# Performance work log

Measured on AMD Instinct MI355X. Metric: run time of the kernel, lower is better.

Reference implementation:

```python
import jax, jax.numpy as jnp
import numpy as np

D_IN = 1024
D_OUT = 1024
NUM_HEADS = 16
HEAD_DIM = D_OUT // NUM_HEADS


def setup_inputs() -> dict:
    key = jax.random.key(0)
    k1, k2, k3, k4 = jax.random.split(key, 4)
    x = jax.random.normal(k1, (2, 2048, D_IN), dtype=jnp.float32)
    # Linear weights stored torch-style [out_features, in_features]
    W_qkv = jax.random.normal(k2, (3 * D_OUT, D_IN), dtype=jnp.float32) * (1.0 / np.sqrt(D_IN))
    W_out = jax.random.normal(k3, (D_OUT, D_OUT), dtype=jnp.float32) * (1.0 / np.sqrt(D_OUT))
    b_out = jax.random.normal(k4, (D_OUT,), dtype=jnp.float32) * 0.01
    return {"x": x, "W_qkv": W_qkv, "W_out": W_out, "b_out": b_out}


def reference(x, W_qkv, W_out, b_out):
    b, s, _ = x.shape
    qkv = jnp.einsum('bsi,oi->bso', x, W_qkv)  # [b, s, 3*d_out]
    q, k, v = jnp.split(qkv, 3, axis=-1)
    def to_heads(t):
        return t.reshape(b, s, NUM_HEADS, HEAD_DIM).transpose(0, 2, 1, 3)
    q, k, v = to_heads(q), to_heads(k), to_heads(v)
    # NOTE: original module does NOT scale by 1/sqrt(head_dim)
    scores = jnp.einsum('bhqd,bhkd->bhqk', q, k)
    causal = jnp.tril(jnp.ones((s, s), dtype=bool))  # True = keep
    scores = jnp.where(causal[None, None], scores, -jnp.inf)
    attn = jax.nn.softmax(scores, axis=-1)
    ctx = jnp.einsum('bhqk,bhkd->bhqd', attn, v)
    ctx = ctx.transpose(0, 2, 1, 3).reshape(b, s, D_OUT)
    return jnp.einsum('bso,po->bsp', ctx, W_out) + b_out
```

## Files before the change

### kernel.cpp

```cpp
#include <hip/hip_runtime.h>
#include <cstdint>
#include <cstddef>


typedef __attribute__((ext_vector_type(8))) short bf16x8;
typedef __attribute__((ext_vector_type(4))) float f32x4;

#define LOG2E 1.44269504f

#define MFMA16(a, b, c) __builtin_amdgcn_mfma_f32_16x16x32_bf16((a), (b), (c), 0, 0, 0)

#define GLDS16(g, s)                                                        \
  __builtin_amdgcn_global_load_lds(                                         \
      (const __attribute__((address_space(1))) void*)(g),                   \
      (__attribute__((address_space(3))) void*)(s), 16, 0, 0)

#if __has_builtin(__builtin_amdgcn_exp2f)
#define EXP2F(x) __builtin_amdgcn_exp2f(x)
#else
#define EXP2F(x) exp2f(x)
#endif

static __device__ __forceinline__ unsigned short f2bf(float f) {
  unsigned int u = __builtin_bit_cast(unsigned int, f);
  u += 0x7FFFu + ((u >> 16) & 1u);
  return (unsigned short)(u >> 16);
}

static __device__ __forceinline__ unsigned int pk2bf(float a, float b) {
  const unsigned int ua = __builtin_bit_cast(unsigned int, a) + 0x8000u;
  const unsigned int ub = __builtin_bit_cast(unsigned int, b) + 0x8000u;
  return __builtin_amdgcn_perm(ub, ua, 0x07060302);
}

__global__ __launch_bounds__(256) void cast_bf16(const float* __restrict__ x,
                                                 const float* __restrict__ wq,
                                                 const float* __restrict__ wo,
                                                 unsigned short* __restrict__ xb,
                                                 unsigned short* __restrict__ wqb,
                                                 unsigned short* __restrict__ wob)
{
  const int id = blockIdx.x * 256 + threadIdx.x;
  const float* src;
  unsigned short* dst;
  int off;
  if (id < 1048576)               { src = x;  dst = xb;  off = id; }
  else if (id < 1048576 + 786432) { src = wq; dst = wqb; off = id - 1048576; }
  else                            { src = wo; dst = wob; off = id - (1048576 + 786432); }
  float4 v = ((const float4*)src)[off];
  ushort4 o;
  o.x = f2bf(v.x); o.y = f2bf(v.y); o.z = f2bf(v.z); o.w = f2bf(v.w);
  ((ushort4*)dst)[off] = o;
}

template <int MODE>
__global__ __launch_bounds__(256) void gemm_bt(const unsigned short* __restrict__ A,
                                               const unsigned short* __restrict__ B,
                                               const float* __restrict__ bias,
                                               float* __restrict__ OutF,
                                               unsigned short* __restrict__ Qb,
                                               unsigned short* __restrict__ Kb,
                                               unsigned short* __restrict__ Vt)
{
  __shared__ unsigned short pool[9216];
  unsigned short* Asm = pool;
  unsigned short* Bsm = pool + 4096;

  const int tid  = threadIdx.x;
  const int wave = tid >> 6, lane = tid & 63, quad = lane >> 4, cl = lane & 15;
  const int wm = wave >> 1, wn = wave & 1;
  const int m0 = blockIdx.y * 128, n0 = blockIdx.x * 128;
  const int sr = lane >> 2, sc = lane & 3;

  f32x4 acc[4][4];
  #pragma unroll
  for (int i = 0; i < 4; ++i)
    #pragma unroll
    for (int j = 0; j < 4; ++j)
      #pragma unroll
      for (int r = 0; r < 4; ++r) acc[i][j][r] = 0.f;

  const int scs = (sc ^ ((sr >> 1) & 3)) * 8;
  const int rchunk = (quad ^ ((cl >> 1) & 3)) * 8;
  for (int k0 = 0; k0 < 1024; k0 += 32) {
    __syncthreads();
    #pragma unroll
    for (int ii = 0; ii < 2; ++ii) {
      const int r = wave * 32 + ii * 16 + sr;
      GLDS16(A + (size_t)(m0 + r) * 1024 + k0 + scs, &Asm[(wave * 32 + ii * 16) * 32]);
      GLDS16(B + (size_t)(n0 + r) * 1024 + k0 + scs, &Bsm[(wave * 32 + ii * 16) * 32]);
    }
    __syncthreads();

    bf16x8 af[4], bfr[4];
    #pragma unroll
    for (int mt = 0; mt < 4; ++mt)
      af[mt] = *(const bf16x8*)&Asm[(wm * 64 + mt * 16 + cl) * 32 + rchunk];
    #pragma unroll
    for (int nt = 0; nt < 4; ++nt)
      bfr[nt] = *(const bf16x8*)&Bsm[(wn * 64 + nt * 16 + cl) * 32 + rchunk];
    #pragma unroll
    for (int mt = 0; mt < 4; ++mt)
      #pragma unroll
      for (int nt = 0; nt < 4; ++nt)
        acc[mt][nt] = MFMA16(af[mt], bfr[nt], acc[mt][nt]);
  }

  if (MODE == 1) {
    const int part = n0 >> 10;
    const int bb = m0 >> 11, ss = m0 & 2047;
    if (part == 2) {
      #pragma unroll
      for (int half = 0; half < 2; ++half) {
        __syncthreads();
        if (wn == half) {
          #pragma unroll
          for (int mt = 0; mt < 4; ++mt)
            #pragma unroll
            for (int nt = 0; nt < 4; ++nt) {
              const int nl = nt * 16 + cl;
              const int ml = wm * 64 + mt * 16 + quad * 4;
              ushort4 pk;
              pk.x = f2bf(acc[mt][nt][0]); pk.y = f2bf(acc[mt][nt][1]);
              pk.z = f2bf(acc[mt][nt][2]); pk.w = f2bf(acc[mt][nt][3]);
              *(ushort4*)&pool[nl * 136 + ml] = pk;
            }
        }
        __syncthreads();
        const int row = tid >> 2, q4 = tid & 3;
        const int nglob = n0 + half * 64 + row;
        const int hh = (nglob >> 6) & 15, d = nglob & 63;
        unsigned short* drow = Vt + ((size_t)(bb * 16 + hh) * 64 + d) * 2048 + ss;
        #pragma unroll
        for (int i = 0; i < 4; ++i) {
          const bf16x8 v = *(const bf16x8*)&pool[row * 136 + q4 * 32 + i * 8];
          *(bf16x8*)(drow + q4 * 32 + i * 8) = v;
        }
      }
    } else {
      unsigned short* dst = (part == 0) ? Qb : Kb;
      const float sc2 = (part == 0) ? LOG2E : 1.0f;
      #pragma unroll
      for (int half = 0; half < 2; ++half) {
        __syncthreads();
        if (wn == half) {
          #pragma unroll
          for (int mt = 0; mt < 4; ++mt)
            #pragma unroll
            for (int nt = 0; nt < 4; ++nt) {
              const int nl = nt * 16 + cl;
              const int ml = wm * 64 + mt * 16 + quad * 4;
              #pragma unroll
              for (int r = 0; r < 4; ++r)
                pool[(ml + r) * 72 + nl] = f2bf(acc[mt][nt][r] * sc2);
            }
        }
        __syncthreads();
        const int m = tid >> 1, dh = (tid & 1) * 32;
        const int hh = ((n0 + half * 64) >> 6) & 15;
        unsigned short* drow = dst + ((size_t)(bb * 16 + hh) * 2048 + ss + m) * 64 + dh;
        #pragma unroll
        for (int i = 0; i < 4; ++i)
          *(bf16x8*)(drow + i * 8) = *(const bf16x8*)&pool[m * 72 + dh + i * 8];
      }
    }
  } else {
    #pragma unroll
    for (int mt = 0; mt < 4; ++mt) {
      const int mbase = m0 + wm * 64 + mt * 16 + quad * 4;
      #pragma unroll
      for (int nt = 0; nt < 4; ++nt) {
        const int n = n0 + wn * 64 + nt * 16 + cl;
        const float bv = bias[n];
        #pragma unroll
        for (int r = 0; r < 4; ++r)
          OutF[(size_t)(mbase + r) * 1024 + n] = acc[mt][nt][r] + bv;
      }
    }
  }
}

__global__ __launch_bounds__(256) void attn_mfma(const unsigned short* __restrict__ Qb,
                                                 const unsigned short* __restrict__ Kb,
                                                 const unsigned short* __restrict__ Vt,
                                                 unsigned short* __restrict__ CTX)
{
  __shared__ unsigned short Ksm[2][64 * 64];
  __shared__ unsigned short Vsm[2][64 * 64];
  __shared__ unsigned short Psm[4][32 * 40];

  const int tid  = threadIdx.x;
  const int wave = tid >> 6, lane = tid & 63, quad = lane >> 4, cl = lane & 15;

  const int L  = blockIdx.x;
  const int bh = 4 * (L & 7) + ((L >> 3) & 3);
  const int b  = bh >> 4, h = bh & 15;
  const int p  = L >> 5;
  const int g  = p * 4 + wave;
  const int qlo = g * 16;
  const int qhi = (127 - g) * 16;
  const size_t base = (size_t)bh * (2048 * 64);

  bf16x8 qf[2][2];
  #pragma unroll
  for (int dk = 0; dk < 2; ++dk) {
    qf[0][dk] = *(const bf16x8*)(Qb + base + (size_t)(qlo + cl) * 64 + dk * 32 + quad * 8);
    qf[1][dk] = *(const bf16x8*)(Qb + base + (size_t)(qhi + cl) * 64 + dk * 32 + quad * 8);
  }

  f32x4 oacc[2][4];
  #pragma unroll
  for (int mf = 0; mf < 2; ++mf)
    #pragma unroll
    for (int dt = 0; dt < 4; ++dt)
      #pragma unroll
      for (int r = 0; r < 4; ++r) oacc[mf][dt][r] = 0.f;
  float lr[2][4] = {};

  bf16x8 ones;
  #pragma unroll
  for (int k = 0; k < 8; ++k) ones[k] = (short)0x3F80;

  const int lrow  = lane >> 3;
  const int lslot = (lane & 7) ^ lrow;
  const int nch = 32 - p;

  #pragma unroll
  for (int ii = 0; ii < 2; ++ii) {
    const int r0 = wave * 16 + ii * 8;
    GLDS16(Kb + base + (size_t)(r0 + lrow) * 64 + lslot * 8, &Ksm[0][r0 * 64]);
    GLDS16(Vt + base + (size_t)(r0 + lrow) * 2048 + lslot * 8, &Vsm[0][r0 * 64]);
  }

  #pragma unroll 1
  for (int ch = 0; ch < nch; ++ch) {
    const int cur = ch & 1;
    __syncthreads();
    if (ch + 1 < nch) {
      const int j64n = (ch + 1) * 64;
      #pragma unroll
      for (int ii = 0; ii < 2; ++ii) {
        const int r0 = wave * 16 + ii * 8;
        GLDS16(Kb + base + (size_t)(j64n + r0 + lrow) * 64 + lslot * 8,
               &Ksm[cur ^ 1][r0 * 64]);
        GLDS16(Vt + base + (size_t)(r0 + lrow) * 2048 + j64n + lslot * 8,
               &Vsm[cur ^ 1][r0 * 64]);
      }
    }

    const int j64 = ch * 64;
    #pragma unroll
    for (int jli = 0; jli < 2; ++jli) {
      const int jg0 = j64 + jli * 32;
      if (jg0 > qhi + 15) continue;
      const bool lowAct = (jg0 <= qlo + 15);
      const int jl = jli * 32;

      bf16x8 kf[2][2];
      #pragma unroll
      for (int jf = 0; jf < 2; ++jf)
        #pragma unroll
        for (int dk = 0; dk < 2; ++dk) {
          const int jrow = jl + jf * 16 + cl;
          const int slot = (dk * 4 + quad) ^ (cl & 7);
          kf[jf][dk] = *(const bf16x8*)&Ksm[cur][jrow * 64 + slot * 8];
        }

      f32x4 st[2][2];
      #pragma unroll
      for (int jf = 0; jf < 2; ++jf)
        #pragma unroll
        for (int mf = 0; mf < 2; ++mf) {
          if (mf == 0 && !lowAct) continue;
          f32x4 z;
          #pragma unroll
          for (int r = 0; r < 4; ++r) z[r] = 0.f;
          z = MFMA16(kf[jf][0], qf[mf][0], z);
          st[jf][mf] = MFMA16(kf[jf][1], qf[mf][1], z);
        }

      #pragma unroll
      for (int mf = 0; mf < 2; ++mf) {
        if (mf == 0 && !lowAct) continue;
        const int qbase = mf ? qhi : qlo;
        const bool diag = (jg0 + 32 > qbase);
        #pragma unroll
        for (int jf = 0; jf < 2; ++jf) {
          float pv[4];
          if (diag) {
            const int qg = qbase + cl;
            #pragma unroll
            for (int r = 0; r < 4; ++r) {
              const int jg = jg0 + jf * 16 + quad * 4 + r;
              pv[r] = (jg <= qg) ? EXP2F(st[jf][mf][r]) : 0.f;
            }
          } else {
            #pragma unroll
            for (int r = 0; r < 4; ++r) pv[r] = EXP2F(st[jf][mf][r]);
          }
          uint2 w;
          w.x = pk2bf(pv[0], pv[1]);
          w.y = pk2bf(pv[2], pv[3]);
          *(uint2*)&Psm[wave][(mf * 16 + cl) * 40 + jf * 16 + quad * 4] = w;
        }
      }

      bf16x8 vf[4];
      #pragma unroll
      for (int dt = 0; dt < 4; ++dt) {
        const int d = dt * 16 + cl;
        const int slot = ((jl >> 3) + quad) ^ (cl & 7);
        vf[dt] = *(const bf16x8*)&Vsm[cur][d * 64 + slot * 8];
      }

      #pragma unroll
      for (int mf = 0; mf < 2; ++mf) {
        if (mf == 0 && !lowAct) continue;
        const bf16x8 pf = *(const bf16x8*)&Psm[wave][(mf * 16 + cl) * 40 + quad * 8];
        f32x4 z;
        #pragma unroll
        for (int r = 0; r < 4; ++r) z[r] = 0.f;
        const f32x4 ls = MFMA16(pf, ones, z);
        #pragma unroll
        for (int r = 0; r < 4; ++r) lr[mf][r] += ls[r];
        #pragma unroll
        for (int dt = 0; dt < 4; ++dt)
          oacc[mf][dt] = MFMA16(pf, vf[dt], oacc[mf][dt]);
      }
    }
  }

  #pragma unroll
  for (int mf = 0; mf < 2; ++mf) {
    const int qbase = mf ? qhi : qlo;
    float inv[4];
    #pragma unroll
    for (int r = 0; r < 4; ++r) inv[r] = 1.f / lr[mf][r];
    #pragma unroll
    for (int dt = 0; dt < 4; ++dt)
      #pragma unroll
      for (int r = 0; r < 4; ++r)
        CTX[(size_t)(b * 2048 + qbase + quad * 4 + r) * 1024 +
            h * 64 + dt * 16 + cl] = f2bf(oacc[mf][dt][r] * inv[r]);
  }
}

extern "C" void kernel_launch(void* const* d_in, const int* in_sizes, int n_in,
                              void* d_out, int out_size, void* d_ws, size_t ws_size,
                              hipStream_t stream)
{
  const float* x    = (const float*)d_in[0];
  const float* Wqkv = (const float*)d_in[1];
  const float* Wout = (const float*)d_in[2];
  const float* bout = (const float*)d_in[3];
  float* out = (float*)d_out;

  char* ws = (char*)d_ws;
  unsigned short* xb  = (unsigned short*)(ws);
  unsigned short* wqb = (unsigned short*)(ws + 8388608);
  unsigned short* wob = (unsigned short*)(ws + 14680064);
  unsigned short* Qb  = (unsigned short*)(ws + 16777216);
  unsigned short* Kb  = (unsigned short*)(ws + 25165824);
  unsigned short* Vt  = (unsigned short*)(ws + 33554432);
  unsigned short* CTX = (unsigned short*)(ws + 41943040);

  cast_bf16<<<dim3(8192), dim3(256), 0, stream>>>(x, Wqkv, Wout, xb, wqb, wob);

  gemm_bt<1><<<dim3(24, 32), dim3(256), 0, stream>>>(xb, wqb, nullptr, nullptr, Qb, Kb, Vt);

  attn_mfma<<<dim3(512), dim3(256), 0, stream>>>(Qb, Kb, Vt, CTX);

  gemm_bt<0><<<dim3(8, 32), dim3(256), 0, stream>>>(CTX, wob, bout, out, nullptr, nullptr, nullptr);
}
```

Baseline: 209.4 us.

## Double-buffer GEMM LDS tiles and swap MFMA operands for vectorized epilogue stores

The GEMM main loop now stages the next K-slice into a second LDS buffer while computing on the current one, removing one barrier per iteration and overlapping global-to-LDS loads with MFMA work. For the output projection and the Q/K parts, the MFMA operands are swapped so each lane holds four consecutive output columns. The epilogue can then write float4/ushort4 directly to global memory instead of going through an LDS transpose with extra barriers. LDS use grows to 32 KB per block, which may reduce occupancy, and the V path keeps the old layout.

Result: faster. 202.6 us (-3.3%).

```diff
diff --git a/kernel.cpp b/kernel.cpp
--- a/kernel.cpp
+++ b/kernel.cpp
@@ -62,9 +62,7 @@
                                                unsigned short* __restrict__ Kb,
                                                unsigned short* __restrict__ Vt)
 {
-  __shared__ unsigned short pool[9216];
-  unsigned short* Asm = pool;
-  unsigned short* Bsm = pool + 4096;
+  __shared__ unsigned short pool[16384];
 
   const int tid  = threadIdx.x;
   const int wave = tid >> 6, lane = tid & 63, quad = lane >> 4, cl = lane & 15;
@@ -72,6 +70,9 @@
   const int m0 = blockIdx.y * 128, n0 = blockIdx.x * 128;
   const int sr = lane >> 2, sc = lane & 3;
 
+  const int part = (MODE == 1) ? (n0 >> 10) : 0;
+  const bool swapped = (MODE == 0) || (part < 2);
+
   f32x4 acc[4][4];
   #pragma unroll
   for (int i = 0; i < 4; ++i)
@@ -82,32 +83,51 @@
 
   const int scs = (sc ^ ((sr >> 1) & 3)) * 8;
   const int rchunk = (quad ^ ((cl >> 1) & 3)) * 8;
-  for (int k0 = 0; k0 < 1024; k0 += 32) {
-    __syncthreads();
+
+  auto stage = [&](int k0, int buf) {
+    unsigned short* As = pool + buf * 4096;
+    unsigned short* Bs = pool + 8192 + buf * 4096;
     #pragma unroll
     for (int ii = 0; ii < 2; ++ii) {
       const int r = wave * 32 + ii * 16 + sr;
-      GLDS16(A + (size_t)(m0 + r) * 1024 + k0 + scs, &Asm[(wave * 32 + ii * 16) * 32]);
-      GLDS16(B + (size_t)(n0 + r) * 1024 + k0 + scs, &Bsm[(wave * 32 + ii * 16) * 32]);
-    }
+      GLDS16(A + (size_t)(m0 + r) * 1024 + k0 + scs, &As[(wave * 32 + ii * 16) * 32]);
+      GLDS16(B + (size_t)(n0 + r) * 1024 + k0 + scs, &Bs[(wave * 32 + ii * 16) * 32]);
+    }
+  };
+
+  stage(0, 0);
+  #pragma unroll 1
+  for (int it = 0; it < 32; ++it) {
+    const int cur = it & 1;
     __syncthreads();
-
+    if (it + 1 < 32) stage((it + 1) * 32, cur ^ 1);
+
+    const unsigned short* As = pool + cur * 4096;
+    const unsigned short* Bs = pool + 8192 + cur * 4096;
     bf16x8 af[4], bfr[4];
     #pragma unroll
     for (int mt = 0; mt < 4; ++mt)
-      af[mt] = *(const bf16x8*)&Asm[(wm * 64 + mt * 16 + cl) * 32 + rchunk];
+      af[mt] = *(const bf16x8*)&As[(wm * 64 + mt * 16 + cl) * 32 + rchunk];
     #pragma unroll
     for (int nt = 0; nt < 4; ++nt)
-      bfr[nt] = *(const bf16x8*)&Bsm[(wn * 64 + nt * 16 + cl) * 32 + rchunk];
-    #pragma unroll
-    for (int mt = 0; mt < 4; ++mt)
-      #pragma unroll
-      for (int nt = 0; nt < 4; ++nt)
-        acc[mt][nt] = MFMA16(af[mt], bfr[nt], acc[mt][nt]);
+      bfr[nt] = *(const bf16x8*)&Bs[(wn * 64 + nt * 16 + cl) * 32 + rchunk];
+
+    if (swapped) {
+      #pragma unroll
+      for (int mt = 0; mt < 4; ++mt)
+        #pragma unroll
+        for (int nt = 0; nt < 4; ++nt)
+          acc[mt][nt] = MFMA16(bfr[nt], af[mt], acc[mt][nt]);
+    } else {
+      #pragma unroll
+      for (int mt = 0; mt < 4; ++mt)
+        #pragma unroll
+        for (int nt = 0; nt < 4; ++nt)
+          acc[mt][nt] = MFMA16(af[mt], bfr[nt], acc[mt][nt]);
+    }
   }
 
   if (MODE == 1) {
-    const int part = n0 >> 10;
     const int bb = m0 >> 11, ss = m0 & 2047;
     if (part == 2) {
       #pragma unroll
@@ -141,40 +161,33 @@
       unsigned short* dst = (part == 0) ? Qb : Kb;
       const float sc2 = (part == 0) ? LOG2E : 1.0f;
       #pragma unroll
-      for (int half = 0; half < 2; ++half) {
-        __syncthreads();
-        if (wn == half) {
-          #pragma unroll
-          for (int mt = 0; mt < 4; ++mt)
-            #pragma unroll
-            for (int nt = 0; nt < 4; ++nt) {
-              const int nl = nt * 16 + cl;
-              const int ml = wm * 64 + mt * 16 + quad * 4;
-              #pragma unroll
-              for (int r = 0; r < 4; ++r)
-                pool[(ml + r) * 72 + nl] = f2bf(acc[mt][nt][r] * sc2);
-            }
-        }
-        __syncthreads();
-        const int m = tid >> 1, dh = (tid & 1) * 32;
-        const int hh = ((n0 + half * 64) >> 6) & 15;
-        unsigned short* drow = dst + ((size_t)(bb * 16 + hh) * 2048 + ss + m) * 64 + dh;
-        #pragma unroll
-        for (int i = 0; i < 4; ++i)
-          *(bf16x8*)(drow + i * 8) = *(const bf16x8*)&pool[m * 72 + dh + i * 8];
+      for (int mt = 0; mt < 4; ++mt) {
+        const int m = ss + wm * 64 + mt * 16 + cl;
+        #pragma unroll
+        for (int nt = 0; nt < 4; ++nt) {
+          const int np = (n0 & 1023) + wn * 64 + nt * 16 + quad * 4;
+          const int hh = np >> 6, d0 = np & 63;
+          ushort4 pk;
+          pk.x = f2bf(acc[mt][nt][0] * sc2);
+          pk.y = f2bf(acc[mt][nt][1] * sc2);
+          pk.z = f2bf(acc[mt][nt][2] * sc2);
+          pk.w = f2bf(acc[mt][nt][3] * sc2);
+          *(ushort4*)&dst[((size_t)(bb * 16 + hh) * 2048 + m) * 64 + d0] = pk;
+        }
       }
     }
   } else {
     #pragma unroll
     for (int mt = 0; mt < 4; ++mt) {
-      const int mbase = m0 + wm * 64 + mt * 16 + quad * 4;
+      const int m = m0 + wm * 64 + mt * 16 + cl;
       #pragma unroll
       for (int nt = 0; nt < 4; ++nt) {
-        const int n = n0 + wn * 64 + nt * 16 + cl;
-        const float bv = bias[n];
-        #pragma unroll
-        for (int r = 0; r < 4; ++r)
-          OutF[(size_t)(mbase + r) * 1024 + n] = acc[mt][nt][r] + bv;
+        const int n = n0 + wn * 64 + nt * 16 + quad * 4;
+        const float4 bv = *(const float4*)(bias + n);
+        float4 o;
+        o.x = acc[mt][nt][0] + bv.x; o.y = acc[mt][nt][1] + bv.y;
+        o.z = acc[mt][nt][2] + bv.z; o.w = acc[mt][nt][3] + bv.w;
+        *(float4*)&OutF[(size_t)m * 1024 + n] = o;
       }
     }
   }
```
